# Kernel optimization log

Measured on AMD Instinct MI355X. Metric: run time of the kernel, lower is better.

## Reference

```python
import jax, jax.numpy as jnp
import numpy as np

BN_EPS = 1e-5


def setup_inputs() -> dict:
    key = jax.random.key(0)
    k1, k2, k3, k4 = jax.random.split(key, 4)
    B, C, D, O, H, W = 8, 21, 64, 128, 256, 256
    return {
        "node_features": jax.random.normal(k1, (B, C, D), dtype=jnp.float32),
        "node_masks": jax.random.uniform(k2, (B, C, H, W), dtype=jnp.float32),
        "conv_w": jax.random.normal(k3, (O, D), dtype=jnp.float32) * 0.05,
        "conv_b": jax.random.normal(k4, (O,), dtype=jnp.float32) * 0.05,
        "gamma": jnp.ones((O,), dtype=jnp.float32),
        "beta": jnp.zeros((O,), dtype=jnp.float32),
    }


def reference(node_features, node_masks, conv_w, conv_b, gamma, beta):
    # Fused scatter-accumulate: equivalent to the B*C python loop of
    # spatial[b] += feat[b,c,:,None,None] * mask[b,c]
    spatial = jnp.einsum("bcd,bchw->bdhw", node_features, node_masks)  # [B,D,H,W]
    # 1x1 conv == per-pixel matmul over channel dim
    y = jnp.einsum("od,bdhw->bohw", conv_w, spatial) + conv_b[None, :, None, None]
    # BatchNorm2d in training mode: batch statistics over (B,H,W), biased var
    mean = jnp.mean(y, axis=(0, 2, 3), keepdims=True)
    var = jnp.mean((y - mean) ** 2, axis=(0, 2, 3), keepdims=True)
    y_hat = (y - mean) * jax.lax.rsqrt(var + BN_EPS)
    out = jax.nn.relu(gamma[None, :, None, None] * y_hat + beta[None, :, None, None])
    return out
```

## Files before the change

### kernel.cpp

```cpp
#include <hip/hip_runtime.h>

#define B_ 8
#define C_ 21
#define D_ 64
#define O_ 128
#define HW_ 65536
#define NTOT_ (B_ * HW_)
#define TRI_N 231
#define GSZ (C_ + TRI_N)
#define NSLOT 32
#define BN_EPS 1e-5

#define OFF_GP 0
#define OFF_P  (B_ * NSLOT * GSZ)
#define OFF_QT (OFF_P + B_ * O_ * C_)
#define OFF_R  (OFF_QT + B_ * O_ * C_)

typedef unsigned short u16;
typedef unsigned int u32;
typedef float nf4 __attribute__((ext_vector_type(4)));
typedef unsigned short nu4 __attribute__((ext_vector_type(4)));
typedef short bf16x8 __attribute__((ext_vector_type(8)));
typedef float f32x16 __attribute__((ext_vector_type(16)));

__device__ __forceinline__ float bf2f(u16 u) {
  return __uint_as_float(((u32)u) << 16);
}
__device__ __forceinline__ u16 f2bf(float f) {
  u32 u = __float_as_uint(f);
  u32 r = u + 0x7FFFu + ((u >> 16) & 1u);
  return (u16)(r >> 16);
}
__device__ __forceinline__ bool is_f32(const void* gamma) {
  return ((const u32*)gamma)[0] == 0x3F800000u;
}

template <bool F32>
__device__ __forceinline__ float ld1(const void* p, size_t i) {
  if (F32) return ((const float*)p)[i];
  return bf2f(((const u16*)p)[i]);
}
template <bool F32>
__device__ __forceinline__ float4 ld4(const void* p, size_t i) {
  if (F32) return *(const float4*)((const float*)p + i);
  ushort4 u = *(const ushort4*)((const u16*)p + i);
  return make_float4(bf2f(u.x), bf2f(u.y), bf2f(u.z), bf2f(u.w));
}
template <bool F32>
__device__ __forceinline__ void st4_nt(void* p, size_t i, float4 v) {
  if (F32) {
    nf4 nv = {v.x, v.y, v.z, v.w};
    __builtin_nontemporal_store(nv, (nf4*)((float*)p + i));
  } else {
    nu4 nv = {f2bf(v.x), f2bf(v.y), f2bf(v.z), f2bf(v.w)};
    __builtin_nontemporal_store(nv, (nu4*)((u16*)p + i));
  }
}

template <bool F32>
__device__ __forceinline__ void kP_impl(const void* feat, const void* w,
                                        float* __restrict__ P, int b, int bx,
                                        int tid) {
  int t = ((bx - 32) * B_ + b) * 256 + tid;
  for (; t < B_ * O_ * C_; t += 8192) {
    int c = t % C_;
    int o = (t / C_) % O_;
    int bb = t / (C_ * O_);
    size_t wo = (size_t)o * D_;
    size_t fo = ((size_t)bb * C_ + c) * D_;
    float acc = 0.f;
#pragma unroll
    for (int i = 0; i < D_; i += 4) {
      float4 a = ld4<F32>(w, wo + i);
      float4 x = ld4<F32>(feat, fo + i);
      acc += a.x * x.x + a.y * x.y + a.z * x.z + a.w * x.w;
    }
    P[t] = acc;
  }
}

__global__ __launch_bounds__(256, 1) void kA_f32(const void* __restrict__ masks,
                                                 const void* __restrict__ feat,
                                                 const void* __restrict__ w,
                                                 const void* __restrict__ gamma,
                                                 float* __restrict__ GP,
                                                 float* __restrict__ P) {
  if (!is_f32(gamma)) return;
  const int b = blockIdx.y, bx = blockIdx.x, tid = threadIdx.x;
  if (bx >= 32) {
    kP_impl<true>(feat, w, P, b, bx, tid);
    return;
  }
  const size_t base = (size_t)b * C_ * HW_;
  float a1[C_], a2[TRI_N];
#pragma unroll
  for (int i = 0; i < C_; ++i) a1[i] = 0.f;
#pragma unroll
  for (int i = 0; i < TRI_N; ++i) a2[i] = 0.f;
  int p = (bx * 256 + tid) * 4;
#pragma unroll 1
  for (int it = 0; it < 2; ++it, p += 32768) {
    float m[C_][4];
#pragma unroll
    for (int c = 0; c < C_; ++c) {
      float4 u = ld4<true>(masks, base + (size_t)c * HW_ + p);
      m[c][0] = u.x; m[c][1] = u.y; m[c][2] = u.z; m[c][3] = u.w;
    }
#pragma unroll
    for (int c = 0; c < C_; ++c) {
#pragma unroll
      for (int k = 0; k < 4; ++k) a1[c] += m[c][k];
#pragma unroll
      for (int cc = c; cc < C_; ++cc) {
        int idx = c * C_ - (c * (c - 1)) / 2 + (cc - c);
#pragma unroll
        for (int k = 0; k < 4; ++k) a2[idx] += m[c][k] * m[cc][k];
      }
    }
  }
#pragma unroll
  for (int off = 32; off > 0; off >>= 1) {
#pragma unroll
    for (int i = 0; i < C_; ++i) a1[i] += __shfl_down(a1[i], off, 64);
#pragma unroll
    for (int i = 0; i < TRI_N; ++i) a2[i] += __shfl_down(a2[i], off, 64);
  }
  __shared__ float g[GSZ];
  for (int i = tid; i < GSZ; i += 256) g[i] = 0.f;
  __syncthreads();
  if ((tid & 63) == 0) {
#pragma unroll
    for (int i = 0; i < C_; ++i) atomicAdd(&g[i], a1[i]);
#pragma unroll
    for (int i = 0; i < TRI_N; ++i) atomicAdd(&g[C_ + i], a2[i]);
  }
  __syncthreads();
  float* slot = GP + ((size_t)b * NSLOT + bx) * GSZ;
  for (int i = tid; i < GSZ; i += 256) slot[i] = g[i];
}

__global__ __launch_bounds__(256) void kA_bf16(const u16* __restrict__ masks,
                                               const void* __restrict__ feat,
                                               const void* __restrict__ w,
                                               const void* __restrict__ gamma,
                                               float* __restrict__ GP,
                                               float* __restrict__ P) {
  if (is_f32(gamma)) return;
  const int b = blockIdx.y, bx = blockIdx.x, tid = threadIdx.x;
  if (bx >= 32) {
    kP_impl<false>(feat, w, P, b, bx, tid);
    return;
  }
  const int wv = tid >> 6;
  const int lane = tid & 63;
  const int row = lane & 31;
  const int kg = lane >> 5;
  const u16* mb = masks + (size_t)b * C_ * HW_;
  const int p0 = (bx * 4 + wv) * 512 + kg * 8;

  const bf16x8 ones8 = {16256, 16256, 16256, 16256, 16256, 16256, 16256, 16256};
  const bf16x8 zero8 = {0, 0, 0, 0, 0, 0, 0, 0};
  f32x16 acc = {0.f, 0.f, 0.f, 0.f, 0.f, 0.f, 0.f, 0.f,
                0.f, 0.f, 0.f, 0.f, 0.f, 0.f, 0.f, 0.f};

  const u16* pr = mb + (size_t)(row < C_ ? row : 0) * HW_ + p0;
#pragma unroll 8
  for (int s = 0; s < 512; s += 16) {
    bf16x8 f;
    if (row < C_)
      f = *(const bf16x8*)(pr + s);
    else if (row == C_)
      f = ones8;
    else
      f = zero8;
    acc = __builtin_amdgcn_mfma_f32_32x32x16_bf16(f, f, acc, 0, 0, 0);
  }

  __shared__ float sG[4][1024];
#pragma unroll
  for (int g = 0; g < 16; ++g) {
    int rr = (g & 3) + 8 * (g >> 2) + 4 * kg;
    sG[wv][rr * 32 + row] = acc[g];
  }
  __syncthreads();
  float* slot = GP + ((size_t)b * NSLOT + bx) * GSZ;
  for (int i = tid; i < GSZ; i += 256) {
    int r, c;
    if (i < C_) {
      r = C_;
      c = i;
    } else {
      int t = i - C_;
      int cr = 0;
      while (t >= C_ - cr) {
        t -= C_ - cr;
        ++cr;
      }
      c = cr;
      r = cr + t;
    }
    int o = r * 32 + c;
    slot[i] = sG[0][o] + sG[1][o] + sG[2][o] + sG[3][o];
  }
}

template <bool F32>
__device__ __forceinline__ void kB_impl(const float* __restrict__ GP,
                                        const float* __restrict__ P,
                                        const void* bias, const void* gamma,
                                        const void* beta, float* __restrict__ Qt,
                                        float* __restrict__ r, int tid) {
  __shared__ float sM[B_ * GSZ];
  for (int idx = tid; idx < B_ * GSZ; idx += 1024) {
    int bb = idx / GSZ, j = idx - bb * GSZ;
    const float* gp = GP + ((size_t)bb * NSLOT) * GSZ + j;
    float s = 0.f;
#pragma unroll
    for (int k = 0; k < NSLOT; ++k) s += gp[k * GSZ];
    sM[idx] = s;
  }
  __syncthreads();
  const int o = tid & (O_ - 1);
  const int b = tid >> 7;
  const float* M1b = sM + b * GSZ;
  const float* M2b = sM + b * GSZ + C_;
  float Pl[C_];
#pragma unroll
  for (int c = 0; c < C_; ++c) Pl[c] = P[(b * O_ + o) * C_ + c];
  double s1 = 0.0, s2 = 0.0;
#pragma unroll
  for (int c = 0; c < C_; ++c) {
    s1 += (double)Pl[c] * (double)M1b[c];
#pragma unroll
    for (int cc = c; cc < C_; ++cc) {
      double m2 = (double)M2b[c * C_ - (c * (c - 1)) / 2 + (cc - c)];
      double term = (double)Pl[c] * (double)Pl[cc] * m2;
      s2 += (cc == c) ? term : 2.0 * term;
    }
  }
  __shared__ double S1s[1024];
  __shared__ double S2s[1024];
  __shared__ float sbc[O_];
  S1s[tid] = s1;
  S2s[tid] = s2;
  __syncthreads();
  if (b == 0) {
    double S1 = 0.0, S2 = 0.0;
#pragma unroll
    for (int bb = 0; bb < B_; ++bb) {
      S1 += S1s[bb * O_ + o];
      S2 += S2s[bb * O_ + o];
    }
    const double N = (double)NTOT_;
    double bi = (double)ld1<F32>(bias, o);
    double mean = bi + S1 / N;
    double ey2 = bi * bi + 2.0 * bi * S1 / N + S2 / N;
    double var = ey2 - mean * mean;
    if (var < 0.0) var = 0.0;
    double inv = 1.0 / sqrt(var + BN_EPS);
    float s = ld1<F32>(gamma, o) * (float)inv;
    sbc[o] = s;
    r[o] = ld1<F32>(beta, o) + s * (float)(bi - mean);
  }
  __syncthreads();
  float s = sbc[o];
#pragma unroll
  for (int c = 0; c < C_; ++c) Qt[((size_t)b * C_ + c) * O_ + o] = s * Pl[c];
}
__global__ __launch_bounds__(1024) void kB(const float* __restrict__ GP,
                                           const float* __restrict__ P,
                                           const void* __restrict__ bias,
                                           const void* __restrict__ gamma,
                                           const void* __restrict__ beta,
                                           float* __restrict__ Qt,
                                           float* __restrict__ r) {
  if (is_f32(gamma)) kB_impl<true>(GP, P, bias, gamma, beta, Qt, r, threadIdx.x);
  else               kB_impl<false>(GP, P, bias, gamma, beta, Qt, r, threadIdx.x);
}

template <bool F32>
__device__ __forceinline__ void kC_impl(const void* masks, const float* __restrict__ Qt,
                                        const float* __restrict__ rv, void* out,
                                        int b, int bx, int tid) {
  const int p0 = (bx * 256 + tid) * 4;
  const size_t mbase = (size_t)b * C_ * HW_ + p0;
  float m[C_][4];
#pragma unroll
  for (int c = 0; c < C_; ++c) {
    float4 u = ld4<F32>(masks, mbase + (size_t)c * HW_);
    m[c][0] = u.x; m[c][1] = u.y; m[c][2] = u.z; m[c][3] = u.w;
  }
  const size_t obase = (size_t)b * O_ * HW_ + p0;
  const float* Qb = Qt + (size_t)b * C_ * O_;
#pragma unroll 1
  for (int oc = 0; oc < O_; oc += 4) {
    const float4 rr = *(const float4*)(rv + oc);
    float acc[4][4];
#pragma unroll
    for (int k = 0; k < 4; ++k) {
      acc[0][k] = rr.x; acc[1][k] = rr.y; acc[2][k] = rr.z; acc[3][k] = rr.w;
    }
#pragma unroll
    for (int c = 0; c < C_; ++c) {
      const float4 q = *(const float4*)(Qb + c * O_ + oc);
#pragma unroll
      for (int k = 0; k < 4; ++k) {
        acc[0][k] = fmaf(q.x, m[c][k], acc[0][k]);
        acc[1][k] = fmaf(q.y, m[c][k], acc[1][k]);
        acc[2][k] = fmaf(q.z, m[c][k], acc[2][k]);
        acc[3][k] = fmaf(q.w, m[c][k], acc[3][k]);
      }
    }
#pragma unroll
    for (int j = 0; j < 4; ++j) {
      float4 v = make_float4(fmaxf(acc[j][0], 0.f), fmaxf(acc[j][1], 0.f),
                             fmaxf(acc[j][2], 0.f), fmaxf(acc[j][3], 0.f));
      st4_nt<F32>(out, obase + (size_t)(oc + j) * HW_, v);
    }
  }
}
__global__ __launch_bounds__(256, 2) void kC(const void* __restrict__ masks,
                                             const float* __restrict__ Qt,
                                             const float* __restrict__ rv,
                                             const void* __restrict__ gamma,
                                             void* __restrict__ out) {
  if (is_f32(gamma)) kC_impl<true>(masks, Qt, rv, out, blockIdx.y, blockIdx.x, threadIdx.x);
  else               kC_impl<false>(masks, Qt, rv, out, blockIdx.y, blockIdx.x, threadIdx.x);
}

extern "C" void kernel_launch(void* const* d_in, const int* in_sizes, int n_in,
                              void* d_out, int out_size, void* d_ws, size_t ws_size,
                              hipStream_t stream) {
  const void* feat  = d_in[0];
  const void* masks = d_in[1];
  const void* w     = d_in[2];
  const void* bias  = d_in[3];
  const void* gamma = d_in[4];
  const void* beta  = d_in[5];
  float* ws = (float*)d_ws;
  float* GP = ws + OFF_GP;
  float* P  = ws + OFF_P;
  float* Qt = ws + OFF_QT;
  float* r  = ws + OFF_R;

  const long long msz = (long long)in_sizes[1];
  const bool skip_f32  = (msz == 22020096LL);
  const bool skip_bf16 = (msz == 44040192LL);
  if (!skip_f32)
    kA_f32<<<dim3(36, B_), dim3(256), 0, stream>>>(masks, feat, w, gamma, GP, P);
  if (!skip_bf16)
    kA_bf16<<<dim3(36, B_), dim3(256), 0, stream>>>((const u16*)masks, feat, w,
                                                    gamma, GP, P);
  kB<<<dim3(1), dim3(1024), 0, stream>>>(GP, P, bias, gamma, beta, Qt, r);
  kC<<<dim3(64, B_), dim3(256), 0, stream>>>(masks, Qt, r, gamma, d_out);
}
```

Baseline: 408.4 us.

## Stage mask tiles through swizzled LDS with register prefetch for Gram MFMA

The Gram-matrix kernel now loads mask data cooperatively into a 21x1024 bf16 LDS tile with XOR swizzling, instead of each lane reading strided global rows directly. It prefetches the second 1024-pixel tile into registers while the MFMAs run on the first, a two-stage software pipeline. The goal is more coalesced global loads and overlap of load latency with compute. The cost is about 43KB of extra LDS plus 11 vector registers per thread, which may lower occupancy, and the per-block pixel coverage per wave is reorganized.

```diff
diff --git a/kernel.cpp b/kernel.cpp
--- a/kernel.cpp
+++ b/kernel.cpp
@@ -155,26 +155,58 @@
   const int lane = tid & 63;
   const int row = lane & 31;
   const int kg = lane >> 5;
-  const u16* mb = masks + (size_t)b * C_ * HW_;
-  const int p0 = (bx * 4 + wv) * 512 + kg * 8;
+
+  __shared__ __align__(16) u16 sm[C_][1024];
+  const u16* mb = masks + (size_t)b * C_ * HW_ + (size_t)bx * 2048;
 
   const bf16x8 ones8 = {16256, 16256, 16256, 16256, 16256, 16256, 16256, 16256};
   const bf16x8 zero8 = {0, 0, 0, 0, 0, 0, 0, 0};
   f32x16 acc = {0.f, 0.f, 0.f, 0.f, 0.f, 0.f, 0.f, 0.f,
                 0.f, 0.f, 0.f, 0.f, 0.f, 0.f, 0.f, 0.f};
 
-  const u16* pr = mb + (size_t)(row < C_ ? row : 0) * HW_ + p0;
-#pragma unroll 8
-  for (int s = 0; s < 512; s += 16) {
-    bf16x8 f;
-    if (row < C_)
-      f = *(const bf16x8*)(pr + s);
-    else if (row == C_)
-      f = ones8;
-    else
-      f = zero8;
-    acc = __builtin_amdgcn_mfma_f32_32x32x16_bf16(f, f, acc, 0, 0, 0);
-  }
+  bf16x8 pf[11];
+#define LOAD_REGS(T)                                                          \
+  _Pragma("unroll") for (int it = 0; it < 11; ++it) {                         \
+    int j = tid + it * 256;                                                   \
+    if (j < C_ * 128)                                                         \
+      pf[it] = *(const bf16x8*)(mb + (size_t)(j >> 7) * HW_ + (T)*1024 +      \
+                                ((j & 127) << 3));                            \
+  }
+#define WRITE_LDS()                                                           \
+  _Pragma("unroll") for (int it = 0; it < 11; ++it) {                         \
+    int j = tid + it * 256;                                                   \
+    if (j < C_ * 128) {                                                       \
+      int r = j >> 7, seg = j & 127;                                          \
+      *(bf16x8*)((char*)sm + r * 2048 + ((seg * 16) ^ ((r & 7) << 4))) =      \
+          pf[it];                                                             \
+    }                                                                         \
+  }
+#define MFMA_TILE()                                                           \
+  _Pragma("unroll") for (int s = 0; s < 16; ++s) {                            \
+    int byteoff = wv * 512 + s * 32 + kg * 16;                                \
+    bf16x8 f;                                                                 \
+    if (row < C_)                                                             \
+      f = *(const bf16x8*)((const char*)sm + row * 2048 +                     \
+                           (byteoff ^ ((row & 7) << 4)));                     \
+    else if (row == C_)                                                       \
+      f = ones8;                                                              \
+    else                                                                      \
+      f = zero8;                                                              \
+    acc = __builtin_amdgcn_mfma_f32_32x32x16_bf16(f, f, acc, 0, 0, 0);        \
+  }
+
+  LOAD_REGS(0);
+  WRITE_LDS();
+  __syncthreads();
+  LOAD_REGS(1);
+  MFMA_TILE();
+  __syncthreads();
+  WRITE_LDS();
+  __syncthreads();
+  MFMA_TILE();
+#undef LOAD_REGS
+#undef WRITE_LDS
+#undef MFMA_TILE
 
   __shared__ float sG[4][1024];
 #pragma unroll
```

After: 480.8 us. 17.7% more time.
